# Kernel tuning notes

Hardware: AMD Instinct MI355X
Metric: run time of the kernel (lower is better)

Reference implementation:

```python
import jax, jax.numpy as jnp
import numpy as np

B, N, E = 8, 10000, 160000
T_IN, T_OUT, C_IN, C_OUT, HID = 12, 12, 2, 2, 128
FLAT = C_IN * T_IN  # 24
EPS = 1e-5  # BatchNorm1d default eps


def setup_inputs() -> dict:
    key = jax.random.key(0)
    ks = jax.random.split(key, 16)
    s = 0.05
    return {
        "x": jax.random.normal(ks[0], (B, T_IN, N, C_IN), jnp.float32),
        "edge_index": jax.random.randint(ks[1], (2, E), 0, N, dtype=jnp.int64),
        "Wl0": jax.random.normal(ks[2], (FLAT, HID), jnp.float32) * s,
        "Wr0": jax.random.normal(ks[3], (FLAT, HID), jnp.float32) * s,
        "bl0": jax.random.normal(ks[4], (HID,), jnp.float32) * s,
        "Wl12": jax.random.normal(ks[5], (2, HID, HID), jnp.float32) * s,
        "Wr12": jax.random.normal(ks[6], (2, HID, HID), jnp.float32) * s,
        "bl12": jax.random.normal(ks[7], (2, HID), jnp.float32) * s,
        "bn_g": jax.random.uniform(ks[8], (3, HID), jnp.float32, 0.5, 1.5),
        "bn_b": jax.random.normal(ks[9], (3, HID), jnp.float32) * s,
        "bn_m": jax.random.normal(ks[10], (3, HID), jnp.float32) * s,
        "bn_v": jax.random.uniform(ks[11], (3, HID), jnp.float32, 0.5, 1.5),
        "head_W": jax.random.normal(ks[12], (HID, T_OUT * C_OUT), jnp.float32) * s,
        "head_b": jax.random.normal(ks[13], (T_OUT * C_OUT,), jnp.float32) * s,
    }


def _sage_conv(h, src, dst, inv_deg, Wl, Wr, bl):
    # PyG SAGEConv (mean aggr): out = lin_l(mean_{j->i} x_j) + lin_r(x_i)
    msg = h[:, src, :]                                   # [B, E, F] gather
    agg = jnp.zeros_like(h).at[:, dst, :].add(msg)       # scatter-add
    mean = agg * inv_deg[None, :, None]                  # mean over neighbors
    return mean @ Wl + bl + h @ Wr


def reference(x, edge_index, Wl0, Wr0, bl0, Wl12, Wr12, bl12,
              bn_g, bn_b, bn_m, bn_v, head_W, head_b):
    src, dst = edge_index[0], edge_index[1]
    deg = jnp.zeros((N,), x.dtype).at[dst].add(1.0)
    inv_deg = 1.0 / jnp.maximum(deg, 1.0)

    # (B, T, N, C) -> (B, N, T*C)
    h = x.transpose(0, 2, 1, 3).reshape(B, N, FLAT)

    layers = [(Wl0, Wr0, bl0), (Wl12[0], Wr12[0], bl12[0]), (Wl12[1], Wr12[1], bl12[1])]
    for i, (Wl, Wr, bl) in enumerate(layers):
        h = _sage_conv(h, src, dst, inv_deg, Wl, Wr, bl)
        # BatchNorm1d in eval mode (running stats); Dropout is identity in eval
        h = (h - bn_m[i]) * (bn_g[i] / jnp.sqrt(bn_v[i] + EPS)) + bn_b[i]
        h = jax.nn.relu(h)

    out = h @ head_W + head_b                            # [B, N, T_out*C_out]
    out = out.reshape(B, N, T_OUT, C_OUT).transpose(0, 2, 1, 3)
    return out                                           # [B, T_out, N, C_out]
```

## Files before the change

### kernel.cpp

```cpp
#include <hip/hip_runtime.h>

#define NB 8
#define NNODE 10000
#define NEDGE 160000
#define MROWS 80000
#define TIN 12
#define EPSBN 1e-5f

typedef __attribute__((ext_vector_type(8))) short bf16x8;
typedef __attribute__((ext_vector_type(4))) float f32x4;
typedef unsigned short u16;
typedef unsigned int u32;

static __device__ __forceinline__ u16 f2bf(float f) {
    unsigned int u = __builtin_bit_cast(unsigned int, f);
    u = (u + 0x7fffu + ((u >> 16) & 1u)) >> 16;
    return (u16)u;
}
static __device__ __forceinline__ float bf2f(u16 h) {
    unsigned int u = ((unsigned int)h) << 16;
    return __builtin_bit_cast(float, u);
}

__global__ __launch_bounds__(256) void fused_pre(const float* __restrict__ x,
                                                 u16* __restrict__ X0,
                                                 const int* __restrict__ ei,
                                                 int* __restrict__ degi,
                                                 const float* __restrict__ Wl0,
                                                 const float* __restrict__ Wr0,
                                                 const float* __restrict__ bl0,
                                                 const float* __restrict__ Wl12,
                                                 const float* __restrict__ Wr12,
                                                 const float* __restrict__ bl12,
                                                 const float* __restrict__ g,
                                                 const float* __restrict__ bb,
                                                 const float* __restrict__ m,
                                                 const float* __restrict__ v,
                                                 u16* __restrict__ W0T, u16* __restrict__ W1T,
                                                 u16* __restrict__ W2T,
                                                 float* __restrict__ bias012) {
    int blk = blockIdx.x;
    if (blk < 313) {
        int row = blk * 256 + threadIdx.x;
        if (row >= MROWS) return;
        int n = row >> 3, b = row & 7;
        u32 w[12];
        #pragma unroll
        for (int tt = 0; tt < 12; ++tt) {
            float2 vv = *(const float2*)&x[(size_t)((b * 12 + tt) * NNODE + n) * 2];
            w[tt] = (u32)f2bf(vv.x) | ((u32)f2bf(vv.y) << 16);
        }
        u32* dst = (u32*)&X0[(size_t)row * 48 + 24];
        *(uint4*)(dst + 0) = make_uint4(w[0], w[1], w[2], w[3]);
        *(uint4*)(dst + 4) = make_uint4(w[4], w[5], w[6], w[7]);
        *(uint4*)(dst + 8) = make_uint4(w[8], w[9], w[10], w[11]);
    } else if (blk < 938) {
        int e = (blk - 313) * 256 + threadIdx.x;
        if (e < NEDGE) atomicAdd(&degi[ei[NEDGE + e]], 1);
    } else {
        int c = blk - 938, k = threadIdx.x;
        float s0 = g[c] / sqrtf(v[c] + EPSBN);
        float s1 = g[128 + c] / sqrtf(v[128 + c] + EPSBN);
        float s2 = g[256 + c] / sqrtf(v[256 + c] + EPSBN);
        if (k < 64) {
            float val = (k < 24) ? Wl0[k * 128 + c] : ((k < 48) ? Wr0[(k - 24) * 128 + c] : 0.0f);
            W0T[c * 64 + k] = f2bf(val * s0);
        }
        float v1 = (k < 128) ? Wl12[k * 128 + c] : Wr12[(k - 128) * 128 + c];
        W1T[c * 256 + k] = f2bf(v1 * s1);
        float v2 = (k < 128) ? Wl12[128 * 128 + k * 128 + c]
                             : Wr12[128 * 128 + (k - 128) * 128 + c];
        W2T[c * 256 + k] = f2bf(v2 * s2);
        if (k < 3) {
            float sl = g[k * 128 + c] / sqrtf(v[k * 128 + c] + EPSBN);
            float blv = (k == 0) ? bl0[c] : bl12[(k - 1) * 128 + c];
            bias012[k * 128 + c] = blv * sl + bb[k * 128 + c] - m[k * 128 + c] * sl;
        }
    }
}

__global__ __launch_bounds__(1024) void scan_kernel(const int* __restrict__ degi,
                                                    int* __restrict__ row_ptr,
                                                    float* __restrict__ inv_deg,
                                                    int* __restrict__ cursor) {
    __shared__ int sdata[1024];
    const int t = threadIdx.x;
    const int CH = 10;
    const int i0 = t * CH;
    int sum = 0;
    for (int i = i0; i < i0 + CH && i < NNODE; ++i) sum += degi[i];
    sdata[t] = sum;
    for (int off = 1; off < 1024; off <<= 1) {
        __syncthreads();
        int vv = (t >= off) ? sdata[t - off] : 0;
        __syncthreads();
        sdata[t] += vv;
    }
    __syncthreads();
    int run = sdata[t] - sum;
    for (int i = i0; i < i0 + CH && i < NNODE; ++i) {
        row_ptr[i] = run;
        int d = degi[i];
        run += d;
        inv_deg[i] = 1.0f / (float)max(d, 1);
        cursor[i] = 0;
    }
    if (t == 1023) row_ptr[NNODE] = sdata[1023];
}

__global__ void csr_fill(const int* __restrict__ ei, const int* __restrict__ row_ptr,
                         int* __restrict__ cursor, int* __restrict__ csr_src) {
    int e = blockIdx.x * blockDim.x + threadIdx.x;
    if (e < NEDGE) {
        int d = ei[NEDGE + e];
        int pos = atomicAdd(&cursor[d], 1);
        csr_src[row_ptr[d] + pos] = ei[e];
    }
}

__global__ __launch_bounds__(192) void agg24(u16* __restrict__ X0,
                                             const int* __restrict__ rp,
                                             const int* __restrict__ cs,
                                             const float* __restrict__ inv) {
    int u = threadIdx.x;
    int n = blockIdx.x * 2 + (u / 96);
    int w = u % 96;
    int b = w / 12, cp = w % 12;
    int p0 = rp[n], p1 = rp[n + 1];
    float a0 = 0, a1 = 0, b0 = 0, b1 = 0, c0 = 0, c1 = 0, d0 = 0, d1 = 0;
    int p = p0;
    for (; p + 4 <= p1; p += 4) {
        int s0 = cs[p], s1 = cs[p + 1], s2 = cs[p + 2], s3 = cs[p + 3];
        u32 v0 = *(const u32*)&X0[(s0 * NB + b) * 48 + 24 + cp * 2];
        u32 v1 = *(const u32*)&X0[(s1 * NB + b) * 48 + 24 + cp * 2];
        u32 v2 = *(const u32*)&X0[(s2 * NB + b) * 48 + 24 + cp * 2];
        u32 v3 = *(const u32*)&X0[(s3 * NB + b) * 48 + 24 + cp * 2];
        a0 += bf2f((u16)(v0 & 0xffff)); a1 += bf2f((u16)(v0 >> 16));
        b0 += bf2f((u16)(v1 & 0xffff)); b1 += bf2f((u16)(v1 >> 16));
        c0 += bf2f((u16)(v2 & 0xffff)); c1 += bf2f((u16)(v2 >> 16));
        d0 += bf2f((u16)(v3 & 0xffff)); d1 += bf2f((u16)(v3 >> 16));
    }
    for (; p < p1; ++p) {
        int s = cs[p];
        u32 vv = *(const u32*)&X0[(s * NB + b) * 48 + 24 + cp * 2];
        a0 += bf2f((u16)(vv & 0xffff)); a1 += bf2f((u16)(vv >> 16));
    }
    float sc = inv[n];
    float r0 = (a0 + b0) + (c0 + d0), r1 = (a1 + b1) + (c1 + d1);
    u32 o = (u32)f2bf(r0 * sc) | ((u32)f2bf(r1 * sc) << 16);
    *(u32*)&X0[(n * NB + b) * 48 + cp * 2] = o;
}

__global__ __launch_bounds__(64) void agg128c(u16* __restrict__ X,
                                              const int* __restrict__ rp,
                                              const int* __restrict__ cs,
                                              const float* __restrict__ inv) {
    int bid = blockIdx.x;
    int c = bid & 7;
    int n = bid >> 3;
    int t = threadIdx.x;
    int b = t >> 3, q = t & 7;
    int p0 = rp[n], p1 = rp[n + 1];
    const u16* hb = X + ((size_t)(8 + c) * MROWS) * 16;
    float a0 = 0, a1 = 0, b0 = 0, b1 = 0, c0 = 0, c1 = 0, d0 = 0, d1 = 0;
    int p = p0;
    for (; p + 4 <= p1; p += 4) {
        int s0 = cs[p], s1 = cs[p + 1], s2 = cs[p + 2], s3 = cs[p + 3];
        u32 v0 = *(const u32*)&hb[(s0 * NB + b) * 16 + q * 2];
        u32 v1 = *(const u32*)&hb[(s1 * NB + b) * 16 + q * 2];
        u32 v2 = *(const u32*)&hb[(s2 * NB + b) * 16 + q * 2];
        u32 v3 = *(const u32*)&hb[(s3 * NB + b) * 16 + q * 2];
        a0 += bf2f((u16)(v0 & 0xffff)); a1 += bf2f((u16)(v0 >> 16));
        b0 += bf2f((u16)(v1 & 0xffff)); b1 += bf2f((u16)(v1 >> 16));
        c0 += bf2f((u16)(v2 & 0xffff)); c1 += bf2f((u16)(v2 >> 16));
        d0 += bf2f((u16)(v3 & 0xffff)); d1 += bf2f((u16)(v3 >> 16));
    }
    for (; p < p1; ++p) {
        int s = cs[p];
        u32 vv = *(const u32*)&hb[(s * NB + b) * 16 + q * 2];
        a0 += bf2f((u16)(vv & 0xffff)); a1 += bf2f((u16)(vv >> 16));
    }
    float sc = inv[n];
    float r0 = (a0 + b0) + (c0 + d0), r1 = (a1 + b1) + (c1 + d1);
    u32 o = (u32)f2bf(r0 * sc) | ((u32)f2bf(r1 * sc) << 16);
    *(u32*)&X[((size_t)c * MROWS + n * NB + b) * 16 + q * 2] = o;
}

#define LOADA(dst, stp) { \
    const int k0_ = (stp) * 32 + kg * 8; \
    _Pragma("unroll") \
    for (int m_ = 0; m_ < 4; ++m_) { \
        const int row_ = rowbase + m_ * 16; \
        const u16* ap_; \
        if (INC) ap_ = A + ((size_t)(k0_ >> 4) * MROWS + row_) * 16 + (k0_ & 15); \
        else     ap_ = A + (size_t)row_ * LDA + k0_; \
        dst[m_] = *(const bf16x8*)ap_; \
    } }

#define MFMAS(av, stp) { \
    const int k0_ = (stp) * 32 + kg * 8; \
    bf16x8 bv_[4]; \
    _Pragma("unroll") \
    for (int n_ = 0; n_ < 4; ++n_) \
        bv_[n_] = *(const bf16x8*)&Bs[wc * 64 + n_ * 16 + r16][k0_]; \
    _Pragma("unroll") \
    for (int m_ = 0; m_ < 4; ++m_) \
        _Pragma("unroll") \
        for (int n_ = 0; n_ < 4; ++n_) \
            acc[m_][n_] = __builtin_amdgcn_mfma_f32_16x16x32_bf16(av[m_], bv_[n_], acc[m_][n_], 0, 0, 0); }

template<int K, int LDA, bool INC, bool HEAD>
__global__ __launch_bounds__(640) void gemm_mfma(const u16* __restrict__ A,
                                                 const u16* __restrict__ WT,
                                                 const float* __restrict__ bias,
                                                 const float* __restrict__ hW,
                                                 const float* __restrict__ hb,
                                                 u16* __restrict__ outc,
                                                 float* __restrict__ outf) {
    constexpr int NSTEP = K / 32;
    constexpr int BS_BYTES = 128 * (K + 8) * 2;
    constexpr int HS_BYTES = 320 * 132 * 2;
    constexpr int SMEM_BYTES = HEAD ? (HS_BYTES + 128 * 24 * 4 + 128) : BS_BYTES;
    __shared__ __align__(16) char smem[SMEM_BYTES];
    typedef short (*BsT)[K + 8];
    BsT Bs = (BsT)smem;

    const int t = threadIdx.x;
    const int row0 = blockIdx.x * 320;
    const int lane = t & 63, wid = t >> 6;
    const int wr = wid >> 1, wc = wid & 1;
    const int r16 = lane & 15, kg = lane >> 4;

    float* Wsf = (float*)(smem + HS_BYTES);
    float* bsh = Wsf + 128 * 24;
    if (HEAD) {
        for (int i = t; i < 128 * 24; i += 640) Wsf[i] = hW[i];
        if (t < 24) bsh[t] = hb[t];
    }
    if (t < 512) {
        const int col = t >> 2, k0 = (t & 3) * (K / 4);
        #pragma unroll
        for (int j = 0; j < K / 32; ++j)
            *(bf16x8*)&Bs[col][k0 + j * 8] =
                *(const bf16x8*)&WT[col * K + k0 + j * 8];
    }
    __syncthreads();

    f32x4 acc[4][4];
    #pragma unroll
    for (int m = 0; m < 4; ++m)
        #pragma unroll
        for (int n = 0; n < 4; ++n)
            acc[m][n] = (f32x4){0.f, 0.f, 0.f, 0.f};

    const int rowbase = row0 + wr * 64 + r16;

    bf16x8 avA[4], avB[4];
    LOADA(avA, 0)
    #pragma unroll
    for (int s2 = 0; s2 < NSTEP; s2 += 2) {
        if (s2 + 1 < NSTEP) LOADA(avB, s2 + 1)
        MFMAS(avA, s2)
        if (s2 + 2 < NSTEP) LOADA(avA, s2 + 2)
        if (s2 + 1 < NSTEP) MFMAS(avB, s2 + 1)
    }

    if (!HEAD) {
        #pragma unroll
        for (int m = 0; m < 4; ++m)
            #pragma unroll
            for (int n = 0; n < 4; ++n) {
                int col = wc * 64 + n * 16 + r16;
                float bvf = bias[col];
                #pragma unroll
                for (int r = 0; r < 4; ++r) {
                    int grow = row0 + wr * 64 + m * 16 + kg * 4 + r;
                    float val = fmaxf(acc[m][n][r] + bvf, 0.0f);
                    outc[((size_t)(8 + wc * 4 + n) * MROWS + grow) * 16 + r16] = f2bf(val);
                }
            }
    } else {
        __syncthreads();
        u16* Hs = (u16*)smem;
        #pragma unroll
        for (int m = 0; m < 4; ++m)
            #pragma unroll
            for (int n = 0; n < 4; ++n) {
                int col = wc * 64 + n * 16 + r16;
                float bvf = bias[col];
                #pragma unroll
                for (int r = 0; r < 4; ++r) {
                    int lrow = wr * 64 + m * 16 + kg * 4 + r;
                    Hs[lrow * 132 + col] = f2bf(fmaxf(acc[m][n][r] + bvf, 0.0f));
                }
            }
        __syncthreads();
        int lrow = t >> 1, half = t & 1;
        const u32* hrow = (const u32*)(Hs + lrow * 132);
        const float* wbase = Wsf + half * 12;
        float a24[12];
        #pragma unroll
        for (int j = 0; j < 12; ++j) a24[j] = bsh[half * 12 + j];
        #pragma unroll 4
        for (int kq = 0; kq < 64; ++kq) {
            u32 wv = hrow[kq];
            float f0 = bf2f((u16)(wv & 0xffff));
            float f1 = bf2f((u16)(wv >> 16));
            const float* w0 = wbase + (kq * 2) * 24;
            #pragma unroll
            for (int j = 0; j < 12; ++j)
                a24[j] = fmaf(f0, w0[j], a24[j]);
            const float* w1 = wbase + (kq * 2 + 1) * 24;
            #pragma unroll
            for (int j = 0; j < 12; ++j)
                a24[j] = fmaf(f1, w1[j], a24[j]);
        }
        int grow = row0 + lrow;
        int n = grow >> 3, b = grow & 7;
        #pragma unroll
        for (int jj = 0; jj < 12; jj += 2) {
            int tt = (half * 12 + jj) >> 1;
            float2 o = {a24[jj], a24[jj + 1]};
            *(float2*)&outf[((size_t)(b * TIN + tt) * NNODE + n) * 2] = o;
        }
    }
}

extern "C" void kernel_launch(void* const* d_in, const int* in_sizes, int n_in,
                              void* d_out, int out_size, void* d_ws, size_t ws_size,
                              hipStream_t stream) {
    const float* x      = (const float*)d_in[0];
    const int*   ei     = (const int*)d_in[1];
    const float* Wl0    = (const float*)d_in[2];
    const float* Wr0    = (const float*)d_in[3];
    const float* bl0    = (const float*)d_in[4];
    const float* Wl12   = (const float*)d_in[5];
    const float* Wr12   = (const float*)d_in[6];
    const float* bl12   = (const float*)d_in[7];
    const float* bn_g   = (const float*)d_in[8];
    const float* bn_b   = (const float*)d_in[9];
    const float* bn_m   = (const float*)d_in[10];
    const float* bn_v   = (const float*)d_in[11];
    const float* headW  = (const float*)d_in[12];
    const float* headb  = (const float*)d_in[13];
    float* out = (float*)d_out;

    u16* X0 = (u16*)d_ws;
    u16* X1 = X0 + (size_t)MROWS * 48 + 32;
    u16* X2 = X1 + (size_t)MROWS * 256;
    u16* W0T = X2 + (size_t)MROWS * 256;
    u16* W1T = W0T + 128 * 64;
    u16* W2T = W1T + 128 * 256;
    float* bias012 = (float*)(W2T + 128 * 256);
    float* inv_deg = bias012 + 3 * 128;
    int* degi    = (int*)(inv_deg + NNODE);
    int* row_ptr = degi + NNODE;
    int* cursor  = row_ptr + (NNODE + 1);
    int* csr_src = cursor + NNODE;

    hipMemsetAsync(degi, 0, sizeof(int) * NNODE, stream);

    fused_pre<<<1066, 256, 0, stream>>>(x, X0, ei, degi, Wl0, Wr0, bl0, Wl12, Wr12,
                                        bl12, bn_g, bn_b, bn_m, bn_v,
                                        W0T, W1T, W2T, bias012);
    scan_kernel<<<1, 1024, 0, stream>>>(degi, row_ptr, inv_deg, cursor);
    csr_fill<<<(NEDGE + 255) / 256, 256, 0, stream>>>(ei, row_ptr, cursor, csr_src);

    agg24<<<NNODE / 2, 192, 0, stream>>>(X0, row_ptr, csr_src, inv_deg);
    gemm_mfma<64, 48, false, false><<<250, 640, 0, stream>>>(X0, W0T, bias012,
                                                             nullptr, nullptr, X1, nullptr);
    agg128c<<<NNODE * 8, 64, 0, stream>>>(X1, row_ptr, csr_src, inv_deg);
    gemm_mfma<256, 0, true, false><<<250, 640, 0, stream>>>(X1, W1T, bias012 + 128,
                                                            nullptr, nullptr, X2, nullptr);
    agg128c<<<NNODE * 8, 64, 0, stream>>>(X2, row_ptr, csr_src, inv_deg);
    gemm_mfma<256, 0, true, true><<<250, 640, 0, stream>>>(X2, W2T, bias012 + 256,
                                                           headW, headb, nullptr, out);
}
```

Measured before the change: 248.5 us.

## Use MFMA for head projection, stage neighbor lists in LDS, reorder B tile layout

The head GEMM (128->24) moves from scalar FP32 FMAs onto bf16 MFMA. The head weights are split into hi/lo bf16 parts so the result keeps near-FP32 precision. The 128-channel aggregation kernel now stages neighbor indices into shared memory and unrolls 8 gathers in flight instead of 4, adding block barriers in exchange. The GEMM's shared B tile is laid out k-major in 8-element chunks to avoid padding and bank conflicts, and the H tile stride changes to 134.

```diff
diff --git a/kernel.cpp b/kernel.cpp
--- a/kernel.cpp
+++ b/kernel.cpp
@@ -36,8 +36,9 @@
                                                  const float* __restrict__ bb,
                                                  const float* __restrict__ m,
                                                  const float* __restrict__ v,
+                                                 const float* __restrict__ hW,
                                                  u16* __restrict__ W0T, u16* __restrict__ W1T,
-                                                 u16* __restrict__ W2T,
+                                                 u16* __restrict__ W2T, u16* __restrict__ W3T,
                                                  float* __restrict__ bias012) {
     int blk = blockIdx.x;
     if (blk < 313) {
@@ -71,6 +72,13 @@
         float v2 = (k < 128) ? Wl12[128 * 128 + k * 128 + c]
                              : Wr12[128 * 128 + (k - 128) * 128 + c];
         W2T[c * 256 + k] = f2bf(v2 * s2);
+        if (k < 128 && c < 64) {
+            int cc = c & 31;
+            float w3 = (cc < 24) ? hW[k * 24 + cc] : 0.0f;
+            u16 hi = f2bf(w3);
+            if (c < 32) W3T[c * 128 + k] = hi;
+            else        W3T[c * 128 + k] = f2bf(w3 - bf2f(hi));
+        }
         if (k < 3) {
             float sl = g[k * 128 + c] / sqrtf(v[k * 128 + c] + EPSBN);
             float blv = (k == 0) ? bl0[c] : bl12[(k - 1) * 128 + c];
@@ -151,10 +159,12 @@
     *(u32*)&X0[(n * NB + b) * 48 + cp * 2] = o;
 }
 
+#define GLD(s) (*(const u32*)&hb[((s) * NB + b) * 16 + q * 2])
 __global__ __launch_bounds__(64) void agg128c(u16* __restrict__ X,
                                               const int* __restrict__ rp,
                                               const int* __restrict__ cs,
                                               const float* __restrict__ inv) {
+    __shared__ int slist[128];
     int bid = blockIdx.x;
     int c = bid & 7;
     int n = bid >> 3;
@@ -163,25 +173,37 @@
     int p0 = rp[n], p1 = rp[n + 1];
     const u16* hb = X + ((size_t)(8 + c) * MROWS) * 16;
     float a0 = 0, a1 = 0, b0 = 0, b1 = 0, c0 = 0, c1 = 0, d0 = 0, d1 = 0;
-    int p = p0;
-    for (; p + 4 <= p1; p += 4) {
-        int s0 = cs[p], s1 = cs[p + 1], s2 = cs[p + 2], s3 = cs[p + 3];
-        u32 v0 = *(const u32*)&hb[(s0 * NB + b) * 16 + q * 2];
-        u32 v1 = *(const u32*)&hb[(s1 * NB + b) * 16 + q * 2];
-        u32 v2 = *(const u32*)&hb[(s2 * NB + b) * 16 + q * 2];
-        u32 v3 = *(const u32*)&hb[(s3 * NB + b) * 16 + q * 2];
-        a0 += bf2f((u16)(v0 & 0xffff)); a1 += bf2f((u16)(v0 >> 16));
-        b0 += bf2f((u16)(v1 & 0xffff)); b1 += bf2f((u16)(v1 >> 16));
-        c0 += bf2f((u16)(v2 & 0xffff)); c1 += bf2f((u16)(v2 >> 16));
-        d0 += bf2f((u16)(v3 & 0xffff)); d1 += bf2f((u16)(v3 >> 16));
-    }
-    for (; p < p1; ++p) {
-        int s = cs[p];
-        u32 vv = *(const u32*)&hb[(s * NB + b) * 16 + q * 2];
-        a0 += bf2f((u16)(vv & 0xffff)); a1 += bf2f((u16)(vv >> 16));
+    float e0 = 0, e1 = 0, f0 = 0, f1 = 0, g0 = 0, g1 = 0, h0 = 0, h1 = 0;
+    for (int base = p0; base < p1; base += 128) {
+        int cnt = p1 - base;
+        if (cnt > 128) cnt = 128;
+        __syncthreads();
+        for (int i = t; i < cnt; i += 64) slist[i] = cs[base + i];
+        __syncthreads();
+        int i = 0;
+        for (; i + 8 <= cnt; i += 8) {
+            int s0 = slist[i + 0], s1 = slist[i + 1], s2 = slist[i + 2], s3 = slist[i + 3];
+            int s4 = slist[i + 4], s5 = slist[i + 5], s6 = slist[i + 6], s7 = slist[i + 7];
+            u32 v0 = GLD(s0), v1 = GLD(s1), v2 = GLD(s2), v3 = GLD(s3);
+            u32 v4 = GLD(s4), v5 = GLD(s5), v6 = GLD(s6), v7 = GLD(s7);
+            a0 += bf2f((u16)(v0 & 0xffff)); a1 += bf2f((u16)(v0 >> 16));
+            b0 += bf2f((u16)(v1 & 0xffff)); b1 += bf2f((u16)(v1 >> 16));
+            c0 += bf2f((u16)(v2 & 0xffff)); c1 += bf2f((u16)(v2 >> 16));
+            d0 += bf2f((u16)(v3 & 0xffff)); d1 += bf2f((u16)(v3 >> 16));
+            e0 += bf2f((u16)(v4 & 0xffff)); e1 += bf2f((u16)(v4 >> 16));
+            f0 += bf2f((u16)(v5 & 0xffff)); f1 += bf2f((u16)(v5 >> 16));
+            g0 += bf2f((u16)(v6 & 0xffff)); g1 += bf2f((u16)(v6 >> 16));
+            h0 += bf2f((u16)(v7 & 0xffff)); h1 += bf2f((u16)(v7 >> 16));
+        }
+        for (; i < cnt; ++i) {
+            int s = slist[i];
+            u32 vv = GLD(s);
+            a0 += bf2f((u16)(vv & 0xffff)); a1 += bf2f((u16)(vv >> 16));
+        }
     }
     float sc = inv[n];
-    float r0 = (a0 + b0) + (c0 + d0), r1 = (a1 + b1) + (c1 + d1);
+    float r0 = ((a0 + b0) + (c0 + d0)) + ((e0 + f0) + (g0 + h0));
+    float r1 = ((a1 + b1) + (c1 + d1)) + ((e1 + f1) + (g1 + h1));
     u32 o = (u32)f2bf(r0 * sc) | ((u32)f2bf(r1 * sc) << 16);
     *(u32*)&X[((size_t)c * MROWS + n * NB + b) * 16 + q * 2] = o;
 }
@@ -202,7 +224,7 @@
     bf16x8 bv_[4]; \
     _Pragma("unroll") \
     for (int n_ = 0; n_ < 4; ++n_) \
-        bv_[n_] = *(const bf16x8*)&Bs[wc * 64 + n_ * 16 + r16][k0_]; \
+        bv_[n_] = *(const bf16x8*)&BsF[(((k0_) >> 3) * 128 + (wc * 64 + n_ * 16 + r16)) * 8]; \
     _Pragma("unroll") \
     for (int m_ = 0; m_ < 4; ++m_) \
         _Pragma("unroll") \
@@ -213,17 +235,17 @@
 __global__ __launch_bounds__(640) void gemm_mfma(const u16* __restrict__ A,
                                                  const u16* __restrict__ WT,
                                                  const float* __restrict__ bias,
-                                                 const float* __restrict__ hW,
+                                                 const u16* __restrict__ W3Tg,
                                                  const float* __restrict__ hb,
                                                  u16* __restrict__ outc,
                                                  float* __restrict__ outf) {
     constexpr int NSTEP = K / 32;
-    constexpr int BS_BYTES = 128 * (K + 8) * 2;
-    constexpr int HS_BYTES = 320 * 132 * 2;
-    constexpr int SMEM_BYTES = HEAD ? (HS_BYTES + 128 * 24 * 4 + 128) : BS_BYTES;
+    constexpr int BS_BYTES = K * 128 * 2;
+    constexpr int HS_BYTES = 320 * 134 * 2;
+    constexpr int W3_BYTES = 64 * 136 * 2;
+    constexpr int SMEM_BYTES = HEAD ? (HS_BYTES + W3_BYTES) : BS_BYTES;
     __shared__ __align__(16) char smem[SMEM_BYTES];
-    typedef short (*BsT)[K + 8];
-    BsT Bs = (BsT)smem;
+    short* BsF = (short*)smem;
 
     const int t = threadIdx.x;
     const int row0 = blockIdx.x * 320;
@@ -231,18 +253,21 @@
     const int wr = wid >> 1, wc = wid & 1;
     const int r16 = lane & 15, kg = lane >> 4;
 
-    float* Wsf = (float*)(smem + HS_BYTES);
-    float* bsh = Wsf + 128 * 24;
+    if (t < 512) {
+        const int col = t >> 2, q = t & 3;
+        #pragma unroll
+        for (int j = 0; j < K / 32; ++j) {
+            int k0 = q * (K / 4) + j * 8;
+            *(bf16x8*)&BsF[((k0 >> 3) * 128 + col) * 8] =
+                *(const bf16x8*)&WT[col * K + k0];
+        }
+    }
     if (HEAD) {
-        for (int i = t; i < 128 * 24; i += 640) Wsf[i] = hW[i];
-        if (t < 24) bsh[t] = hb[t];
-    }
-    if (t < 512) {
-        const int col = t >> 2, k0 = (t & 3) * (K / 4);
-        #pragma unroll
-        for (int j = 0; j < K / 32; ++j)
-            *(bf16x8*)&Bs[col][k0 + j * 8] =
-                *(const bf16x8*)&WT[col * K + k0 + j * 8];
+        short* W3 = (short*)(smem + HS_BYTES);
+        for (int i = t; i < 1024; i += 640) {
+            int row = i >> 4, j = i & 15;
+            *(bf16x8*)&W3[row * 136 + j * 8] = *(const bf16x8*)&W3Tg[row * 128 + j * 8];
+        }
     }
     __syncthreads();
 
@@ -282,6 +307,7 @@
     } else {
         __syncthreads();
         u16* Hs = (u16*)smem;
+        short* W3 = (short*)(smem + HS_BYTES);
         #pragma unroll
         for (int m = 0; m < 4; ++m)
             #pragma unroll
@@ -291,38 +317,50 @@
                 #pragma unroll
                 for (int r = 0; r < 4; ++r) {
                     int lrow = wr * 64 + m * 16 + kg * 4 + r;
-                    Hs[lrow * 132 + col] = f2bf(fmaxf(acc[m][n][r] + bvf, 0.0f));
+                    Hs[lrow * 134 + col] = f2bf(fmaxf(acc[m][n][r] + bvf, 0.0f));
                 }
             }
         __syncthreads();
-        int lrow = t >> 1, half = t & 1;
-        const u32* hrow = (const u32*)(Hs + lrow * 132);
-        const float* wbase = Wsf + half * 12;
-        float a24[12];
-        #pragma unroll
-        for (int j = 0; j < 12; ++j) a24[j] = bsh[half * 12 + j];
-        #pragma unroll 4
-        for (int kq = 0; kq < 64; ++kq) {
-            u32 wv = hrow[kq];
-            float f0 = bf2f((u16)(wv & 0xffff));
-            float f1 = bf2f((u16)(wv >> 16));
-            const float* w0 = wbase + (kq * 2) * 24;
-            #pragma unroll
-            for (int j = 0; j < 12; ++j)
-                a24[j] = fmaf(f0, w0[j], a24[j]);
-            const float* w1 = wbase + (kq * 2 + 1) * 24;
-            #pragma unroll
-            for (int j = 0; j < 12; ++j)
-                a24[j] = fmaf(f1, w1[j], a24[j]);
-        }
-        int grow = row0 + lrow;
-        int n = grow >> 3, b = grow & 7;
-        #pragma unroll
-        for (int jj = 0; jj < 12; jj += 2) {
-            int tt = (half * 12 + jj) >> 1;
-            float2 o = {a24[jj], a24[jj + 1]};
-            *(float2*)&outf[((size_t)(b * TIN + tt) * NNODE + n) * 2] = o;
-        }
+        f32x4 hacc[2][4];
+        #pragma unroll
+        for (int m = 0; m < 2; ++m)
+            #pragma unroll
+            for (int n = 0; n < 4; ++n)
+                hacc[m][n] = (f32x4){0.f, 0.f, 0.f, 0.f};
+        #pragma unroll
+        for (int ks = 0; ks < 4; ++ks) {
+            const int k0 = ks * 32 + kg * 8;
+            bf16x8 ha[2], hbv[4];
+            #pragma unroll
+            for (int m = 0; m < 2; ++m)
+                ha[m] = *(const bf16x8*)&Hs[(wid * 32 + m * 16 + r16) * 134 + k0];
+            #pragma unroll
+            for (int n = 0; n < 4; ++n)
+                hbv[n] = *(const bf16x8*)&W3[(n * 16 + r16) * 136 + k0];
+            #pragma unroll
+            for (int m = 0; m < 2; ++m)
+                #pragma unroll
+                for (int n = 0; n < 4; ++n)
+                    hacc[m][n] = __builtin_amdgcn_mfma_f32_16x16x32_bf16(
+                        ha[m], hbv[n], hacc[m][n], 0, 0, 0);
+        }
+        #pragma unroll
+        for (int m = 0; m < 2; ++m)
+            #pragma unroll
+            for (int nt = 0; nt < 2; ++nt) {
+                int col = nt * 16 + r16;
+                if (col < 24) {
+                    float hbias = hb[col];
+                    int tt = col >> 1, cc = col & 1;
+                    #pragma unroll
+                    for (int r = 0; r < 4; ++r) {
+                        int grow = row0 + wid * 32 + m * 16 + kg * 4 + r;
+                        float val = hacc[m][nt][r] + hacc[m][nt + 2][r] + hbias;
+                        int n = grow >> 3, b = grow & 7;
+                        outf[((size_t)(b * TIN + tt) * NNODE + n) * 2 + cc] = val;
+                    }
+                }
+            }
     }
 }
 
@@ -351,7 +389,8 @@
     u16* W0T = X2 + (size_t)MROWS * 256;
     u16* W1T = W0T + 128 * 64;
     u16* W2T = W1T + 128 * 256;
-    float* bias012 = (float*)(W2T + 128 * 256);
+    u16* W3T = W2T + 128 * 256;
+    float* bias012 = (float*)(W3T + 64 * 128);
     float* inv_deg = bias012 + 3 * 128;
     int* degi    = (int*)(inv_deg + NNODE);
     int* row_ptr = degi + NNODE;
@@ -361,8 +400,8 @@
     hipMemsetAsync(degi, 0, sizeof(int) * NNODE, stream);
 
     fused_pre<<<1066, 256, 0, stream>>>(x, X0, ei, degi, Wl0, Wr0, bl0, Wl12, Wr12,
-                                        bl12, bn_g, bn_b, bn_m, bn_v,
-                                        W0T, W1T, W2T, bias012);
+                                        bl12, bn_g, bn_b, bn_m, bn_v, headW,
+                                        W0T, W1T, W2T, W3T, bias012);
     scan_kernel<<<1, 1024, 0, stream>>>(degi, row_ptr, inv_deg, cursor);
     csr_fill<<<(NEDGE + 255) / 256, 256, 0, stream>>>(ei, row_ptr, cursor, csr_src);
 
@@ -374,5 +413,5 @@
                                                             nullptr, nullptr, X2, nullptr);
     agg128c<<<NNODE * 8, 64, 0, stream>>>(X2, row_ptr, csr_src, inv_deg);
     gemm_mfma<256, 0, true, true><<<250, 640, 0, stream>>>(X2, W2T, bias012 + 256,
-                                                           headW, headb, nullptr, out);
-}
+                                                           W3T, headb, nullptr, out);
+}
```

New measurement: 250.5 us. No clear change (+0.8%).
